# Optimization experiments

Hardware: AMD Instinct MI355X
Metric: run time of the kernel (lower is better)

## Reference

```python
import jax, jax.numpy as jnp
import numpy as np

B, LQ, NB, NT = 4, 512, 32, 256
D_MODEL, N_HEADS, D_K, D_V = 512, 8, 64, 64
SCALE = 1.0 / np.sqrt(D_K).astype(np.float32)


def setup_inputs() -> dict:
    key = jax.random.key(0)
    ks = jax.random.split(key, 16)
    std = 0.02
    p = lambda k, shp: (std * jax.random.normal(k, shp, dtype=jnp.float32))
    return {
        'q':   jax.random.normal(ks[0], (B, LQ, D_MODEL), dtype=jnp.float32),
        'k_w': jax.random.normal(ks[1], (B, NB, NT, D_MODEL), dtype=jnp.float32),
        'v_w': jax.random.normal(ks[2], (B, NB, NT, D_MODEL), dtype=jnp.float32),
        'k_s': jax.random.normal(ks[3], (B, NB, D_MODEL), dtype=jnp.float32),
        'v_s': jax.random.normal(ks[4], (B, NB, D_MODEL), dtype=jnp.float32),
        'W_qs': p(ks[5], (D_MODEL, N_HEADS * D_K)), 'b_qs': jnp.zeros((N_HEADS * D_K,), jnp.float32),
        'W_ks': p(ks[6], (D_MODEL, N_HEADS * D_K)), 'b_ks': jnp.zeros((N_HEADS * D_K,), jnp.float32),
        'W_vs': p(ks[7], (D_MODEL, N_HEADS * D_V)), 'b_vs': jnp.zeros((N_HEADS * D_V,), jnp.float32),
        'W_qw': p(ks[8], (D_MODEL, N_HEADS * D_K)), 'b_qw': jnp.zeros((N_HEADS * D_K,), jnp.float32),
        'W_kw': p(ks[9], (D_MODEL, N_HEADS * D_K)), 'b_kw': jnp.zeros((N_HEADS * D_K,), jnp.float32),
        'W_vw': p(ks[10], (D_MODEL, N_HEADS * D_V)), 'b_vw': jnp.zeros((N_HEADS * D_V,), jnp.float32),
        'W_fc1': p(ks[11], (N_HEADS * D_V, D_MODEL)), 'b_fc1': jnp.zeros((D_MODEL,), jnp.float32),
        'W_fc':  p(ks[12], (D_MODEL + N_HEADS * D_V, D_MODEL)), 'b_fc': jnp.zeros((D_MODEL,), jnp.float32),
    }


def reference(q, k_w, v_w, k_s, v_s,
              W_qs, b_qs, W_ks, b_ks, W_vs, b_vs,
              W_qw, b_qw, W_kw, b_kw, W_vw, b_vw,
              W_fc1, b_fc1, W_fc, b_fc):
    b, lq = q.shape[0], q.shape[1]
    nb, nt = k_w.shape[1], k_w.shape[2]
    h, dk, dv = N_HEADS, D_K, D_V

    # ---- sentence-level (graph) attention ----
    qs = (q @ W_qs + b_qs).reshape(b, lq, h, dk)        # [b,lq,h,dk]
    ks_ = (k_s @ W_ks + b_ks).reshape(b, nb, h, dk)     # [b,nb,h,dk]
    vs_ = (v_s @ W_vs + b_vs).reshape(b, nb, h, dv)     # [b,nb,h,dv]
    attn_s = jnp.einsum('bqhd,bnhd->bhqn', qs * SCALE, ks_)  # [b,h,lq,nb]
    attn_s = jax.nn.softmax(attn_s, axis=-1)
    ctx_s = jnp.einsum('bhqn,bnhd->bqhd', attn_s, vs_).reshape(b, lq, h * dv)
    ctx_s = ctx_s @ W_fc1 + b_fc1                        # [b,lq,d_model]

    # ---- token-level attention with sentence norm ----
    qw = (q @ W_qw + b_qw).reshape(b, lq, h, dk)         # [b,lq,h,dk]
    kw = (k_w @ W_kw + b_kw).reshape(b, nb, nt, h, dk)
    vw = (v_w @ W_vw + b_vw).reshape(b, nb, nt, h, dv)
    attn_w = jnp.einsum('bqhd,bnthd->bhqnt', qw * SCALE, kw)  # [b,h,lq,nb,nt]
    wts = jax.nn.softmax(attn_w, axis=-1)                # softmax over tokens within each block
    aw = wts * attn_s[..., None]                         # sentence-weighted token attention
    ctx_w = jnp.einsum('bhqnt,bnthd->bqhd', aw, vw).reshape(b, lq, h * dv)

    out = jnp.concatenate([ctx_s, ctx_w], axis=-1) @ W_fc + b_fc  # [b,lq,d_model]
    return out
```

## Files before the change

### kernel.cpp

```cpp
#include <hip/hip_runtime.h>
#include <hip/hip_bf16.h>

#define SCALE_F 0.125f

typedef __attribute__((ext_vector_type(8))) short short8;
typedef __attribute__((ext_vector_type(4))) float f32x4;
typedef __attribute__((address_space(3))) void lds_void;
typedef const __attribute__((address_space(1))) void glb_void;

__device__ __forceinline__ unsigned short f2b(float f){
  return __builtin_bit_cast(unsigned short, __float2bfloat16(f));
}
__device__ __forceinline__ float b2f(unsigned short h){
  return __uint_as_float((unsigned int)h << 16);
}

template<int MODE>
__device__ __forceinline__ void sgemm_body(
    unsigned short* sm, const float* __restrict__ A,
    const float* __restrict__ p0, const float* __restrict__ p1,
    const float* __restrict__ W, const float* __restrict__ bias,
    float* __restrict__ outf, float scale, int m0, int n0, int K, int tid)
{
  unsigned short* Ah = sm;
  unsigned short* Al = sm + 4096;
  unsigned short* Bh = sm + 8192;
  unsigned short* Bl = sm + 12288;
  const int lane = tid & 63, wv = tid >> 6, lr = lane & 15, lg = lane >> 4;

  f32x4 acc[4];
  #pragma unroll
  for (int nf = 0; nf < 4; nf++) acc[nf] = (f32x4){0.f, 0.f, 0.f, 0.f};

  for (int k0 = 0; k0 < K; k0 += 64) {
    float4 a0[2], a1[2];
    float bw[2][8];
    const bool dual = (MODE == 1) && (k0 >= 512);
    const int kk = dual ? (k0 - 512) : k0;
    #pragma unroll
    for (int j = 0; j < 2; j++) {
      int idx = tid + j * 256;
      int row = idx >> 3, c8 = idx & 7;
      size_t base = (size_t)(m0 + row) * 512 + kk + c8 * 8;
      if (dual) {
        float4 x0 = *(const float4*)&p0[base];
        float4 x1 = *(const float4*)&p0[base + 4];
        float4 y0 = *(const float4*)&p1[base];
        float4 y1 = *(const float4*)&p1[base + 4];
        a0[j] = (float4){x0.x + y0.x, x0.y + y0.y, x0.z + y0.z, x0.w + y0.w};
        a1[j] = (float4){x1.x + y1.x, x1.y + y1.y, x1.z + y1.z, x1.w + y1.w};
      } else {
        a0[j] = *(const float4*)&A[base];
        a1[j] = *(const float4*)&A[base + 4];
      }
    }
    #pragma unroll
    for (int j = 0; j < 2; j++) {
      int idx = tid + j * 256;
      int nl = idx >> 3, kseg = idx & 7;
      #pragma unroll
      for (int e = 0; e < 8; e++)
        bw[j][e] = W[(size_t)(k0 + kseg * 8 + e) * 512 + n0 + nl];
    }
    __syncthreads();
    #pragma unroll
    for (int j = 0; j < 2; j++) {
      int idx = tid + j * 256;
      int row = idx >> 3, c8 = idx & 7;
      int off = row * 64 + ((c8 * 8) ^ ((row & 7) << 3));
      float v[8] = {a0[j].x, a0[j].y, a0[j].z, a0[j].w,
                    a1[j].x, a1[j].y, a1[j].z, a1[j].w};
      short8 h, l;
      #pragma unroll
      for (int e = 0; e < 8; e++) {
        unsigned short hh = f2b(v[e]);
        h[e] = (short)hh;
        l[e] = (short)f2b(v[e] - b2f(hh));
      }
      *(short8*)&Ah[off] = h;
      *(short8*)&Al[off] = l;
    }
    #pragma unroll
    for (int j = 0; j < 2; j++) {
      int idx = tid + j * 256;
      int nl = idx >> 3, kseg = idx & 7;
      int off = nl * 64 + ((kseg * 8) ^ ((nl & 7) << 3));
      short8 h, l;
      #pragma unroll
      for (int e = 0; e < 8; e++) {
        unsigned short hh = f2b(bw[j][e]);
        h[e] = (short)hh;
        l[e] = (short)f2b(bw[j][e] - b2f(hh));
      }
      *(short8*)&Bh[off] = h;
      *(short8*)&Bl[off] = l;
    }
    __syncthreads();
    #pragma unroll
    for (int ks = 0; ks < 2; ks++) {
      int rowa = wv * 16 + lr;
      int aoff = rowa * 64 + ((ks * 32 + lg * 8) ^ ((rowa & 7) << 3));
      short8 ah = *(const short8*)&Ah[aoff];
      short8 al = *(const short8*)&Al[aoff];
      #pragma unroll
      for (int nf = 0; nf < 4; nf++) {
        int rowb = nf * 16 + lr;
        int boff = rowb * 64 + ((ks * 32 + lg * 8) ^ ((rowb & 7) << 3));
        short8 bh = *(const short8*)&Bh[boff];
        short8 bl = *(const short8*)&Bl[boff];
        acc[nf] = __builtin_amdgcn_mfma_f32_16x16x32_bf16(ah, bh, acc[nf], 0, 0, 0);
        acc[nf] = __builtin_amdgcn_mfma_f32_16x16x32_bf16(ah, bl, acc[nf], 0, 0, 0);
        acc[nf] = __builtin_amdgcn_mfma_f32_16x16x32_bf16(al, bh, acc[nf], 0, 0, 0);
      }
    }
  }

  #pragma unroll
  for (int nf = 0; nf < 4; nf++) {
    int n = n0 + nf * 16 + lr;
    float bv = bias[n];
    #pragma unroll
    for (int i = 0; i < 4; i++) {
      int m = m0 + wv * 16 + lg * 4 + i;
      float v = (acc[nf][i] + bv) * scale;
      if (MODE == 0 || MODE == 1) {
        outf[(size_t)m * 512 + n] = v;
      } else if (MODE == 2) {
        int bb = m >> 9, qq = m & 511, hh = n >> 6, d = n & 63;
        outf[((((size_t)bb * 8 + hh) * 512 + qq) << 6) + d] = v;
      } else {
        int bb = m >> 5, nn = m & 31, hh = n >> 6, d = n & 63;
        outf[((((size_t)bb * 8 + hh) * 32 + nn) << 6) + d] = v;
      }
    }
  }
}

template<int VT>
__device__ __forceinline__ void proj_epilogue(
    f32x4 (&acc)[4][4], const float* __restrict__ bias,
    __hip_bfloat16* __restrict__ outW, int m0, int n0,
    int wr, int wc, int lr, int lg)
{
  #pragma unroll
  for (int nj = 0; nj < 4; nj++) {
    int n = n0 + wc * 64 + nj * 16 + lr;
    float bv = bias[n];
    int hh = n >> 6, d = n & 63;
    #pragma unroll
    for (int mi = 0; mi < 4; mi++) {
      if (VT == 0) {
        #pragma unroll
        for (int i = 0; i < 4; i++) {
          int m = m0 + wr * 64 + mi * 16 + lg * 4 + i;
          int bb = m >> 13, r = m & 8191, nn = r >> 8, tt = r & 255;
          outW[(((((size_t)bb * 8 + hh) * 32 + nn) * 256 + tt) << 6) + d] =
              __float2bfloat16(acc[mi][nj][i] + bv);
        }
      } else {
        int m = m0 + wr * 64 + mi * 16 + lg * 4;
        int bb = m >> 13, r = m & 8191, nn = r >> 8, t0 = r & 255;
        uint2 pk;
        pk.x = (unsigned)f2b(acc[mi][nj][0] + bv) | ((unsigned)f2b(acc[mi][nj][1] + bv) << 16);
        pk.y = (unsigned)f2b(acc[mi][nj][2] + bv) | ((unsigned)f2b(acc[mi][nj][3] + bv) << 16);
        *(uint2*)((unsigned short*)outW +
                  (((((size_t)bb * 8 + hh) * 32 + nn) * 64 + d) << 8) + t0) = pk;
      }
    }
  }
}

template<int VT>
__device__ __forceinline__ void proj_reg(
    unsigned short* sm, const float* __restrict__ A,
    const unsigned short* __restrict__ BT, const float* __restrict__ bias,
    __hip_bfloat16* __restrict__ outW, int bidLocal, int tid)
{
  unsigned short* As = sm;
  unsigned short* Bs = sm + 8192;
  const int xcd = bidLocal & 7, local = bidLocal >> 3;
  const int mx = xcd * 32 + (local >> 2);
  const int ny = local & 3;
  const int m0 = mx * 128, n0 = ny * 128;
  const int lane = tid & 63, wv = tid >> 6, lr = lane & 15, lg = lane >> 4;
  const int wr = wv >> 1, wc = wv & 1;

  f32x4 acc[4][4];
  #pragma unroll
  for (int mi = 0; mi < 4; mi++)
    #pragma unroll
    for (int nj = 0; nj < 4; nj++) acc[mi][nj] = (f32x4){0.f, 0.f, 0.f, 0.f};

  for (int k0 = 0; k0 < 512; k0 += 64) {
    float4 a0[4], a1[4]; uint4 bq[4];
    #pragma unroll
    for (int j = 0; j < 4; j++) {
      int idx = tid + j * 256;
      int row = idx >> 3, c8 = idx & 7;
      const float* ap = A + (size_t)(m0 + row) * 512 + k0 + c8 * 8;
      a0[j] = *(const float4*)ap;
      a1[j] = *(const float4*)(ap + 4);
      bq[j] = *(const uint4*)(BT + (size_t)(n0 + row) * 512 + k0 + c8 * 8);
    }
    __syncthreads();
    #pragma unroll
    for (int j = 0; j < 4; j++) {
      int idx = tid + j * 256;
      int row = idx >> 3, c8 = idx & 7;
      int off = row * 64 + ((c8 * 8) ^ ((row & 7) << 3));
      short8 pk;
      pk[0] = (short)f2b(a0[j].x); pk[1] = (short)f2b(a0[j].y);
      pk[2] = (short)f2b(a0[j].z); pk[3] = (short)f2b(a0[j].w);
      pk[4] = (short)f2b(a1[j].x); pk[5] = (short)f2b(a1[j].y);
      pk[6] = (short)f2b(a1[j].z); pk[7] = (short)f2b(a1[j].w);
      *(short8*)&As[off] = pk;
      *(uint4*)&Bs[off] = bq[j];
    }
    __syncthreads();
    #pragma unroll
    for (int ks = 0; ks < 2; ks++) {
      short8 af[4], bfp[4];
      #pragma unroll
      for (int mi = 0; mi < 4; mi++) {
        int row = wr * 64 + mi * 16 + lr;
        af[mi] = *(const short8*)&As[row * 64 + ((ks * 32 + lg * 8) ^ ((row & 7) << 3))];
      }
      #pragma unroll
      for (int nj = 0; nj < 4; nj++) {
        int row = wc * 64 + nj * 16 + lr;
        bfp[nj] = *(const short8*)&Bs[row * 64 + ((ks * 32 + lg * 8) ^ ((row & 7) << 3))];
      }
      #pragma unroll
      for (int mi = 0; mi < 4; mi++)
        #pragma unroll
        for (int nj = 0; nj < 4; nj++)
          acc[mi][nj] = __builtin_amdgcn_mfma_f32_16x16x32_bf16(af[mi], bfp[nj], acc[mi][nj], 0, 0, 0);
    }
  }
  proj_epilogue<VT>(acc, bias, outW, m0, n0, wr, wc, lr, lg);
}

template<int VT>
__device__ __forceinline__ void proj_glds(
    unsigned short* sm, const unsigned short* __restrict__ Abf,
    const unsigned short* __restrict__ BT, const float* __restrict__ bias,
    __hip_bfloat16* __restrict__ outW, int bidLocal, int tid)
{
  unsigned short* As = sm;
  unsigned short* Bs = sm + 8192;
  const int xcd = bidLocal & 7, local = bidLocal >> 3;
  const int mx = xcd * 32 + (local >> 2);
  const int ny = local & 3;
  const int m0 = mx * 128, n0 = ny * 128;
  const int lane = tid & 63, wv = tid >> 6, lr = lane & 15, lg = lane >> 4;
  const int wr = wv >> 1, wc = wv & 1;
  const int srow = tid >> 3, scc = tid & 7;

  f32x4 acc[4][4];
  #pragma unroll
  for (int mi = 0; mi < 4; mi++)
    #pragma unroll
    for (int nj = 0; nj < 4; nj++) acc[mi][nj] = (f32x4){0.f, 0.f, 0.f, 0.f};

  for (int k0 = 0; k0 < 512; k0 += 64) {
    __syncthreads();
    #pragma unroll
    for (int issue = 0; issue < 4; issue++) {
      int row = issue * 32 + srow;
      int cs = (scc ^ (row & 7)) * 8;
      const unsigned short* ga = Abf + (size_t)(m0 + row) * 512 + k0 + cs;
      const unsigned short* gb = BT  + (size_t)(n0 + row) * 512 + k0 + cs;
      unsigned short* la = As + issue * 2048 + wv * 512;
      unsigned short* lb = Bs + issue * 2048 + wv * 512;
      __builtin_amdgcn_global_load_lds((glb_void*)ga, (lds_void*)la, 16, 0, 0);
      __builtin_amdgcn_global_load_lds((glb_void*)gb, (lds_void*)lb, 16, 0, 0);
    }
    asm volatile("s_waitcnt vmcnt(0)" ::: "memory");
    __syncthreads();
    #pragma unroll
    for (int ks = 0; ks < 2; ks++) {
      short8 af[4], bfp[4];
      #pragma unroll
      for (int mi = 0; mi < 4; mi++) {
        int row = wr * 64 + mi * 16 + lr;
        af[mi] = *(const short8*)&As[row * 64 + ((ks * 32 + lg * 8) ^ ((row & 7) << 3))];
      }
      #pragma unroll
      for (int nj = 0; nj < 4; nj++) {
        int row = wc * 64 + nj * 16 + lr;
        bfp[nj] = *(const short8*)&Bs[row * 64 + ((ks * 32 + lg * 8) ^ ((row & 7) << 3))];
      }
      #pragma unroll
      for (int mi = 0; mi < 4; mi++)
        #pragma unroll
        for (int nj = 0; nj < 4; nj++)
          acc[mi][nj] = __builtin_amdgcn_mfma_f32_16x16x32_bf16(af[mi], bfp[nj], acc[mi][nj], 0, 0, 0);
    }
  }
  proj_epilogue<VT>(acc, bias, outW, m0, n0, wr, wc, lr, lg);
}

__device__ __forceinline__ void tok_body(
    unsigned short* sm, const float* __restrict__ qw,
    const __hip_bfloat16* __restrict__ kw, const __hip_bfloat16* __restrict__ vwT,
    const float* __restrict__ attn_s, float* __restrict__ part0,
    float* __restrict__ part1, int bid, int tid)
{
  unsigned short* kvbuf = sm;
  unsigned short* pbuf  = sm + 18432;
  const int xcd = bid & 7, slot = bid >> 3;
  const int bh = xcd * 4 + (slot >> 4);
  const int rest = slot & 15;
  const int qt = rest >> 1, z = rest & 1;
  const int b = bh >> 3, h = bh & 7;
  const int wv = tid >> 6, lane = tid & 63, lg = lane >> 4, lr = lane & 15;
  const int qbase = qt * 64 + wv * 16;
  const int n0 = z * 16;
  const int vd = wv * 16 + (lane >> 2), tq = lane & 3;

  short8 qfrag[2];
  {
    const float* qrow = qw + ((size_t)bh * 512 + qbase + lr) * 64;
    #pragma unroll
    for (int ks = 0; ks < 2; ks++) {
      float4 u0 = *(const float4*)&qrow[ks * 32 + lg * 8];
      float4 u1 = *(const float4*)&qrow[ks * 32 + lg * 8 + 4];
      short8 t;
      t[0] = f2b(u0.x); t[1] = f2b(u0.y); t[2] = f2b(u0.z); t[3] = f2b(u0.w);
      t[4] = f2b(u1.x); t[5] = f2b(u1.y); t[6] = f2b(u1.z); t[7] = f2b(u1.w);
      qfrag[ks] = t;
    }
  }
  float asv[16];
  {
    const float* ap = attn_s + ((size_t)bh * 512 + qbase + lr) * 32 + n0;
    #pragma unroll
    for (int i = 0; i < 4; i++) {
      float4 u = *(const float4*)&ap[i * 4];
      asv[i * 4 + 0] = u.x; asv[i * 4 + 1] = u.y;
      asv[i * 4 + 2] = u.z; asv[i * 4 + 3] = u.w;
    }
  }

  f32x4 acc[4];
  #pragma unroll
  for (int dt = 0; dt < 4; dt++) acc[dt] = (f32x4){0.f, 0.f, 0.f, 0.f};

  const unsigned short* kwb = (const unsigned short*)kw + (size_t)bh * 32 * 256 * 64;
  const unsigned short* vtb = (const unsigned short*)vwT + (size_t)bh * 32 * 64 * 256;
  const unsigned int pbase = (wv * 16 + lr) * 264;

  for (int ni = 0; ni < 16; ni++) {
    const int n = n0 + ni;
    __syncthreads();
    {
      const unsigned short* ksrc = kwb + ((size_t)n * 256 + tid) * 64;
      uint4 r[8];
      #pragma unroll
      for (int j = 0; j < 8; j++) r[j] = *(const uint4*)(ksrc + j * 8);
      #pragma unroll
      for (int j = 0; j < 8; j++) *(uint4*)&kvbuf[tid * 72 + j * 8] = r[j];
    }
    __syncthreads();

    f32x4 sfr[16];
    #pragma unroll
    for (int tt = 0; tt < 16; tt++) sfr[tt] = (f32x4){0.f, 0.f, 0.f, 0.f};
    __builtin_amdgcn_s_setprio(1);
    #pragma unroll
    for (int tt = 0; tt < 16; tt++) {
      #pragma unroll
      for (int ks = 0; ks < 2; ks++) {
        short8 kf = *(const short8*)&kvbuf[(16 * tt + lr) * 72 + ks * 32 + lg * 8];
        sfr[tt] = __builtin_amdgcn_mfma_f32_16x16x32_bf16(kf, qfrag[ks], sfr[tt], 0, 0, 0);
      }
    }
    __builtin_amdgcn_s_setprio(0);
    float lsum = 0.f;
    #pragma unroll
    for (int tt = 0; tt < 16; tt++) {
      #pragma unroll
      for (int i = 0; i < 4; i++) {
        float e = __expf(sfr[tt][i]);
        sfr[tt][i] = e;
        lsum += e;
      }
    }
    lsum += __shfl_xor(lsum, 16);
    lsum += __shfl_xor(lsum, 32);
    const float coef = asv[ni] / lsum;
    #pragma unroll
    for (int tt = 0; tt < 16; tt++) {
      uint2 pk;
      pk.x = (unsigned)f2b(sfr[tt][0] * coef) | ((unsigned)f2b(sfr[tt][1] * coef) << 16);
      pk.y = (unsigned)f2b(sfr[tt][2] * coef) | ((unsigned)f2b(sfr[tt][3] * coef) << 16);
      *(uint2*)&pbuf[pbase + tt * 16 + lg * 4] = pk;
    }
    __syncthreads();

    {
      const unsigned short* vsrc = vtb + ((size_t)n * 64 + vd) * 256 + tq * 64;
      uint4 r[8];
      #pragma unroll
      for (int j = 0; j < 8; j++) r[j] = *(const uint4*)(vsrc + j * 8);
      #pragma unroll
      for (int j = 0; j < 8; j++)
        *(uint4*)&kvbuf[vd * 264 + tq * 64 + ((j ^ tq) * 8)] = r[j];
    }
    __syncthreads();

    __builtin_amdgcn_s_setprio(1);
    #pragma unroll
    for (int ks = 0; ks < 8; ks++) {
      short8 pa = *(const short8*)&pbuf[pbase + ks * 32 + lg * 8];
      const int tqe = ks >> 1, joff = (ks & 1) * 4 + lg;
      #pragma unroll
      for (int dt = 0; dt < 4; dt++) {
        short8 vb = *(const short8*)&kvbuf[(16 * dt + lr) * 264 + tqe * 64 + ((joff ^ tqe) * 8)];
        acc[dt] = __builtin_amdgcn_mfma_f32_16x16x32_bf16(pa, vb, acc[dt], 0, 0, 0);
      }
    }
    __builtin_amdgcn_s_setprio(0);
  }

  float* pout = z ? part1 : part0;
  #pragma unroll
  for (int dt = 0; dt < 4; dt++) {
    #pragma unroll
    for (int i = 0; i < 4; i++) {
      int qg = qt * 64 + wv * 16 + lg * 4 + i;
      pout[((size_t)b * 512 + qg) * 512 + h * 64 + dt * 16 + lr] = acc[dt][i];
    }
  }
}

__global__ __launch_bounds__(256)
void prep(const float* __restrict__ kwf, const float* __restrict__ vwf,
          unsigned short* __restrict__ kbf, unsigned short* __restrict__ vbf,
          const float* __restrict__ W0, unsigned short* __restrict__ T0,
          const float* __restrict__ W1, unsigned short* __restrict__ T1,
          int ncast)
{
  __shared__ unsigned short tile[64][72];
  const int bid = blockIdx.x, tid = threadIdx.x;
  if (bid < 2 * ncast) {
    const float* src = (bid < ncast) ? kwf : vwf;
    unsigned short* dst = (bid < ncast) ? kbf : vbf;
    size_t off = (size_t)((bid < ncast) ? bid : bid - ncast) * 8192;
    #pragma unroll
    for (int i = 0; i < 8; i++) {
      size_t idx = off + ((size_t)i * 256 + tid) * 4;
      float4 v = *(const float4*)&src[idx];
      uint2 pk;
      pk.x = (unsigned)f2b(v.x) | ((unsigned)f2b(v.y) << 16);
      pk.y = (unsigned)f2b(v.z) | ((unsigned)f2b(v.w) << 16);
      *(uint2*)&dst[idx] = pk;
    }
  } else {
    int local = bid - 2 * ncast;
    const float* W = (local >> 6) ? W1 : W0;
    unsigned short* T = (local >> 6) ? T1 : T0;
    int k0 = (local & 7) * 64, n0 = ((local >> 3) & 7) * 64;
    #pragma unroll
    for (int j = 0; j < 16; j++) {
      int idx = tid + j * 256;
      int r = idx >> 6, c = idx & 63;
      tile[r][c] = f2b(W[(size_t)(k0 + r) * 512 + n0 + c]);
    }
    __syncthreads();
    #pragma unroll
    for (int j = 0; j < 16; j++) {
      int idx = tid + j * 256;
      int r = idx >> 6, c = idx & 63;
      T[(size_t)(n0 + r) * 512 + k0 + c] = tile[c][r];
    }
  }
}

__global__ __launch_bounds__(256)
void megaA_glds(const float* __restrict__ q,
           const unsigned short* __restrict__ kbf, const unsigned short* __restrict__ vbf,
           const float* __restrict__ k_s, const float* __restrict__ v_s,
           const float* __restrict__ W_qs, const float* __restrict__ b_qs,
           const float* __restrict__ W_qw, const float* __restrict__ b_qw,
           const float* __restrict__ W_ks, const float* __restrict__ b_ks,
           const float* __restrict__ W_vs, const float* __restrict__ b_vs,
           const unsigned short* __restrict__ WkT, const float* __restrict__ b_kw,
           const unsigned short* __restrict__ WvT, const float* __restrict__ b_vw,
           float* qs_ws, float* qw_ws, float* ks_ws, float* vs_ws,
           __hip_bfloat16* kw_ws, __hip_bfloat16* vwT_ws)
{
  __shared__ unsigned short sm[16384];
  const int bid = blockIdx.x, tid = threadIdx.x;
  if (bid < 1024) {
    proj_glds<0>(sm, kbf, WkT, b_kw, kw_ws, bid, tid);
  } else if (bid < 2048) {
    proj_glds<1>(sm, vbf, WvT, b_vw, vwT_ws, bid - 1024, tid);
  } else if (bid < 2560) {
    int local = bid - 2048;
    int bx = local & 31, by = (local >> 5) & 7, bz = local >> 8;
    if (bz == 0)
      sgemm_body<2>(sm, q, nullptr, nullptr, W_qs, b_qs, qs_ws, SCALE_F, bx * 64, by * 64, 512, tid);
    else
      sgemm_body<2>(sm, q, nullptr, nullptr, W_qw, b_qw, qw_ws, SCALE_F, bx * 64, by * 64, 512, tid);
  } else {
    int local = bid - 2560;
    int bx = local & 1, by = (local >> 1) & 7, bz = local >> 4;
    if (bz == 0)
      sgemm_body<3>(sm, k_s, nullptr, nullptr, W_ks, b_ks, ks_ws, 1.f, bx * 64, by * 64, 512, tid);
    else
      sgemm_body<3>(sm, v_s, nullptr, nullptr, W_vs, b_vs, vs_ws, 1.f, bx * 64, by * 64, 512, tid);
  }
}

__global__ __launch_bounds__(256)
void megaA_reg(const float* __restrict__ q,
           const float* __restrict__ k_w, const float* __restrict__ v_w,
           const float* __restrict__ k_s, const float* __restrict__ v_s,
           const float* __restrict__ W_qs, const float* __restrict__ b_qs,
           const float* __restrict__ W_qw, const float* __restrict__ b_qw,
           const float* __restrict__ W_ks, const float* __restrict__ b_ks,
           const float* __restrict__ W_vs, const float* __restrict__ b_vs,
           const unsigned short* __restrict__ WkT, const float* __restrict__ b_kw,
           const unsigned short* __restrict__ WvT, const float* __restrict__ b_vw,
           float* qs_ws, float* qw_ws, float* ks_ws, float* vs_ws,
           __hip_bfloat16* kw_ws, __hip_bfloat16* vwT_ws)
{
  __shared__ unsigned short sm[16384];
  const int bid = blockIdx.x, tid = threadIdx.x;
  if (bid < 1024) {
    proj_reg<0>(sm, k_w, WkT, b_kw, kw_ws, bid, tid);
  } else if (bid < 2048) {
    proj_reg<1>(sm, v_w, WvT, b_vw, vwT_ws, bid - 1024, tid);
  } else if (bid < 2560) {
    int local = bid - 2048;
    int bx = local & 31, by = (local >> 5) & 7, bz = local >> 8;
    if (bz == 0)
      sgemm_body<2>(sm, q, nullptr, nullptr, W_qs, b_qs, qs_ws, SCALE_F, bx * 64, by * 64, 512, tid);
    else
      sgemm_body<2>(sm, q, nullptr, nullptr, W_qw, b_qw, qw_ws, SCALE_F, bx * 64, by * 64, 512, tid);
  } else {
    int local = bid - 2560;
    int bx = local & 1, by = (local >> 1) & 7, bz = local >> 4;
    if (bz == 0)
      sgemm_body<3>(sm, k_s, nullptr, nullptr, W_ks, b_ks, ks_ws, 1.f, bx * 64, by * 64, 512, tid);
    else
      sgemm_body<3>(sm, v_s, nullptr, nullptr, W_vs, b_vs, vs_ws, 1.f, bx * 64, by * 64, 512, tid);
  }
}

__global__ __launch_bounds__(256, 2)
void megaB(const float* __restrict__ qw,
           const __hip_bfloat16* __restrict__ kw, const __hip_bfloat16* __restrict__ vwT,
           const float* __restrict__ attn_s, float* part0, float* part1,
           const float* __restrict__ ctxs,
           const float* __restrict__ W_fc1, const float* __restrict__ b_fc1,
           float* ctxsf)
{
  __shared__ unsigned short sm[35328];
  const int bid = blockIdx.x, tid = threadIdx.x;
  if (bid < 512) {
    tok_body(sm, qw, kw, vwT, attn_s, part0, part1, bid, tid);
  } else {
    int local = bid - 512;
    sgemm_body<0>(sm, ctxs, nullptr, nullptr, W_fc1, b_fc1, ctxsf, 1.f,
                  (local & 31) * 64, (local >> 5) * 64, 512, tid);
  }
}

__global__ __launch_bounds__(256)
void final_gemm(const float* __restrict__ ctxsf,
                const float* __restrict__ p0, const float* __restrict__ p1,
                const float* __restrict__ W, const float* __restrict__ bias,
                float* out)
{
  __shared__ unsigned short sm[16384];
  sgemm_body<1>(sm, ctxsf, p0, p1, W, bias, out, 1.f,
                blockIdx.x * 64, blockIdx.y * 64, 1024, threadIdx.x);
}

__global__ __launch_bounds__(256)
void sent_attn(const float* __restrict__ qs,
               const float* __restrict__ ks,
               const float* __restrict__ vs,
               float* __restrict__ attn_s,
               float* __restrict__ ctx_s)
{
  __shared__ float qsS[32][68];
  __shared__ float ksS[32][68];
  __shared__ float vsS[32][68];
  __shared__ float sS[32][36];
  const int bh = blockIdx.y, b = bh >> 3, h = bh & 7;
  const int q0 = blockIdx.x * 32;
  const int tid = threadIdx.x;

  #pragma unroll
  for (int i = 0; i < 2; i++) {
    int idx = tid + i * 256;
    int r = idx >> 4, c = (idx & 15) * 4;
    *(float4*)&qsS[r][c] = *(const float4*)&qs[((size_t)bh * 512 + q0 + r) * 64 + c];
    *(float4*)&ksS[r][c] = *(const float4*)&ks[((size_t)bh * 32 + r) * 64 + c];
    *(float4*)&vsS[r][c] = *(const float4*)&vs[((size_t)bh * 32 + r) * 64 + c];
  }
  __syncthreads();

  #pragma unroll
  for (int it = 0; it < 4; it++) {
    int pair = tid + it * 256;
    int qq = pair >> 5, nn = pair & 31;
    float s = 0.f;
    #pragma unroll
    for (int k = 0; k < 64; k++) s += qsS[qq][k] * ksS[nn][k];
    sS[qq][nn] = s;
  }
  __syncthreads();

  if (tid < 32) {
    int qq = tid;
    float m = -1e30f;
    #pragma unroll
    for (int n = 0; n < 32; n++) m = fmaxf(m, sS[qq][n]);
    float p[32];
    float sum = 0.f;
    #pragma unroll
    for (int n = 0; n < 32; n++) { p[n] = __expf(sS[qq][n] - m); sum += p[n]; }
    float inv = 1.f / sum;
    #pragma unroll
    for (int n = 0; n < 32; n++) {
      float pv = p[n] * inv;
      sS[qq][n] = pv;
      attn_s[((size_t)bh * 512 + q0 + qq) * 32 + n] = pv;
    }
  }
  __syncthreads();

  #pragma unroll
  for (int it = 0; it < 8; it++) {
    int idx = tid + it * 256;
    int qq = idx >> 6, d = idx & 63;
    float c = 0.f;
    #pragma unroll
    for (int n = 0; n < 32; n++) c += sS[qq][n] * vsS[n][d];
    ctx_s[((size_t)b * 512 + q0 + qq) * 512 + h * 64 + d] = c;
  }
}

extern "C" void kernel_launch(void* const* d_in, const int* in_sizes, int n_in,
                              void* d_out, int out_size, void* d_ws, size_t ws_size,
                              hipStream_t stream)
{
  (void)in_sizes; (void)n_in; (void)out_size;
  const float* q    = (const float*)d_in[0];
  const float* k_w  = (const float*)d_in[1];
  const float* v_w  = (const float*)d_in[2];
  const float* k_s  = (const float*)d_in[3];
  const float* v_s  = (const float*)d_in[4];
  const float* W_qs = (const float*)d_in[5];  const float* b_qs = (const float*)d_in[6];
  const float* W_ks = (const float*)d_in[7];  const float* b_ks = (const float*)d_in[8];
  const float* W_vs = (const float*)d_in[9];  const float* b_vs = (const float*)d_in[10];
  const float* W_qw = (const float*)d_in[11]; const float* b_qw = (const float*)d_in[12];
  const float* W_kw = (const float*)d_in[13]; const float* b_kw = (const float*)d_in[14];
  const float* W_vw = (const float*)d_in[15]; const float* b_vw = (const float*)d_in[16];
  const float* W_fc1= (const float*)d_in[17]; const float* b_fc1= (const float*)d_in[18];
  const float* W_fc = (const float*)d_in[19]; const float* b_fc = (const float*)d_in[20];
  float* out = (float*)d_out;

  char* ws = (char*)d_ws;
  const size_t MB = 1ull << 20;
  const size_t KB = 1ull << 10;
  float* qs_ws    = (float*)(ws + 0 * MB);
  float* qw_ws    = (float*)(ws + 4 * MB);
  float* ks_ws    = (float*)(ws + 8 * MB);
  unsigned short* WkT = (unsigned short*)(ws + 8 * MB + 512 * KB);
  float* vs_ws    = (float*)(ws + 9 * MB);
  unsigned short* WvT = (unsigned short*)(ws + 9 * MB + 512 * KB);
  float* attns_ws = (float*)(ws + 10 * MB);
  float* ctxs_ws  = (float*)(ws + 12 * MB);
  float* ctxsf_ws = (float*)(ws + 16 * MB);
  float* part1    = (float*)(ws + 20 * MB);
  __hip_bfloat16* kw_ws  = (__hip_bfloat16*)(ws + 24 * MB);
  __hip_bfloat16* vwT_ws = (__hip_bfloat16*)(ws + 56 * MB);
  unsigned short* kbf = (unsigned short*)(ws + 88 * MB);
  unsigned short* vbf = (unsigned short*)(ws + 120 * MB);
  float* part0    = (float*)(ws + 0 * MB);

  const bool use_glds = (ws_size >= 152ull * MB);
  const int ncast = use_glds ? 2048 : 0;

  dim3 blk(256);
  prep<<<dim3(2 * ncast + 128), blk, 0, stream>>>(
      k_w, v_w, kbf, vbf, W_kw, WkT, W_vw, WvT, ncast);
  if (use_glds) {
    megaA_glds<<<dim3(2592), blk, 0, stream>>>(
        q, kbf, vbf, k_s, v_s,
        W_qs, b_qs, W_qw, b_qw, W_ks, b_ks, W_vs, b_vs,
        WkT, b_kw, WvT, b_vw,
        qs_ws, qw_ws, ks_ws, vs_ws, kw_ws, vwT_ws);
  } else {
    megaA_reg<<<dim3(2592), blk, 0, stream>>>(
        q, k_w, v_w, k_s, v_s,
        W_qs, b_qs, W_qw, b_qw, W_ks, b_ks, W_vs, b_vs,
        WkT, b_kw, WvT, b_vw,
        qs_ws, qw_ws, ks_ws, vs_ws, kw_ws, vwT_ws);
  }
  sent_attn<<<dim3(16, 32), blk, 0, stream>>>(qs_ws, ks_ws, vs_ws, attns_ws, ctxs_ws);
  megaB<<<dim3(768), blk, 0, stream>>>(
      qw_ws, kw_ws, vwT_ws, attns_ws, part0, part1,
      ctxs_ws, W_fc1, b_fc1, ctxsf_ws);
  final_gemm<<<dim3(32, 8), blk, 0, stream>>>(ctxsf_ws, part0, part1, W_fc, b_fc, out);
}
```

Baseline: 271.1 us.

## Regroup kernels: fold small projections into cast prep, sentence attention into K/V projection

The q/k_s/v_s projections move out of the big K/V projection kernel into the first prep kernel, next to the bf16 casts and the weight transposes. Sentence attention, which only depends on those projections, now runs as extra blocks inside the K/V projection kernel, so one launch disappears. Separately, the token-attention LDS buffers switch from padded rows to XOR-swizzled unpadded layouts, which shrinks megaB shared memory to 64KB and aims to avoid bank conflicts. The risks are load imbalance from the heterogeneous block mixes and correctness of the new swizzle indexing.

```diff
diff --git a/kernel.cpp b/kernel.cpp
--- a/kernel.cpp
+++ b/kernel.cpp
@@ -300,6 +300,69 @@
   proj_epilogue<VT>(acc, bias, outW, m0, n0, wr, wc, lr, lg);
 }
 
+__device__ __forceinline__ void sent_body(
+    float* smf, const float* __restrict__ qs, const float* __restrict__ ks,
+    const float* __restrict__ vs, float* __restrict__ attn_s,
+    float* __restrict__ ctx_s, int bidLocal, int tid)
+{
+  float* qsS = smf;
+  float* ksS = smf + 2176;
+  float* vsS = smf + 4352;
+  float* sS  = smf + 6528;
+  const int bh = bidLocal >> 4, b = bh >> 3, h = bh & 7;
+  const int q0 = (bidLocal & 15) * 32;
+
+  #pragma unroll
+  for (int i = 0; i < 2; i++) {
+    int idx = tid + i * 256;
+    int r = idx >> 4, c = (idx & 15) * 4;
+    *(float4*)&qsS[r * 68 + c] = *(const float4*)&qs[((size_t)bh * 512 + q0 + r) * 64 + c];
+    *(float4*)&ksS[r * 68 + c] = *(const float4*)&ks[((size_t)bh * 32 + r) * 64 + c];
+    *(float4*)&vsS[r * 68 + c] = *(const float4*)&vs[((size_t)bh * 32 + r) * 64 + c];
+  }
+  __syncthreads();
+
+  #pragma unroll
+  for (int it = 0; it < 4; it++) {
+    int pair = tid + it * 256;
+    int qq = pair >> 5, nn = pair & 31;
+    float s = 0.f;
+    #pragma unroll
+    for (int k = 0; k < 64; k++) s += qsS[qq * 68 + k] * ksS[nn * 68 + k];
+    sS[qq * 36 + nn] = s;
+  }
+  __syncthreads();
+
+  if (tid < 32) {
+    int qq = tid;
+    float m = -1e30f;
+    #pragma unroll
+    for (int n = 0; n < 32; n++) m = fmaxf(m, sS[qq * 36 + n]);
+    float p[32];
+    float sum = 0.f;
+    #pragma unroll
+    for (int n = 0; n < 32; n++) { p[n] = __expf(sS[qq * 36 + n] - m); sum += p[n]; }
+    float inv = 1.f / sum;
+    #pragma unroll
+    for (int n = 0; n < 32; n++) {
+      float pv = p[n] * inv;
+      sS[qq * 36 + n] = pv;
+      attn_s[((size_t)bh * 512 + q0 + qq) * 32 + n] = pv;
+    }
+  }
+  __syncthreads();
+
+  #pragma unroll
+  for (int it = 0; it < 8; it++) {
+    int idx = tid + it * 256;
+    int qq = idx >> 6, d = idx & 63;
+    float c = 0.f;
+    #pragma unroll
+    for (int n = 0; n < 32; n++) c += sS[qq * 36 + n] * vsS[n * 68 + d];
+    ctx_s[((size_t)b * 512 + q0 + qq) * 512 + h * 64 + d] = c;
+  }
+}
+
 __device__ __forceinline__ void tok_body(
     unsigned short* sm, const float* __restrict__ qw,
     const __hip_bfloat16* __restrict__ kw, const __hip_bfloat16* __restrict__ vwT,
@@ -307,7 +370,7 @@
     float* __restrict__ part1, int bid, int tid)
 {
   unsigned short* kvbuf = sm;
-  unsigned short* pbuf  = sm + 18432;
+  unsigned short* pbuf  = sm + 16384;
   const int xcd = bid & 7, slot = bid >> 3;
   const int bh = xcd * 4 + (slot >> 4);
   const int rest = slot & 15;
@@ -317,6 +380,8 @@
   const int qbase = qt * 64 + wv * 16;
   const int n0 = z * 16;
   const int vd = wv * 16 + (lane >> 2), tq = lane & 3;
+  const int swz = (lr & 7) << 3;
+  const int vswz = (vd & 7) << 3;
 
   short8 qfrag[2];
   {
@@ -348,7 +413,7 @@
 
   const unsigned short* kwb = (const unsigned short*)kw + (size_t)bh * 32 * 256 * 64;
   const unsigned short* vtb = (const unsigned short*)vwT + (size_t)bh * 32 * 64 * 256;
-  const unsigned int pbase = (wv * 16 + lr) * 264;
+  const unsigned int prow = (wv * 16 + lr) * 256;
 
   for (int ni = 0; ni < 16; ni++) {
     const int n = n0 + ni;
@@ -359,7 +424,8 @@
       #pragma unroll
       for (int j = 0; j < 8; j++) r[j] = *(const uint4*)(ksrc + j * 8);
       #pragma unroll
-      for (int j = 0; j < 8; j++) *(uint4*)&kvbuf[tid * 72 + j * 8] = r[j];
+      for (int j = 0; j < 8; j++)
+        *(uint4*)&kvbuf[tid * 64 + (((j << 3)) ^ ((tid & 7) << 3))] = r[j];
     }
     __syncthreads();
 
@@ -371,7 +437,7 @@
     for (int tt = 0; tt < 16; tt++) {
       #pragma unroll
       for (int ks = 0; ks < 2; ks++) {
-        short8 kf = *(const short8*)&kvbuf[(16 * tt + lr) * 72 + ks * 32 + lg * 8];
+        short8 kf = *(const short8*)&kvbuf[(16 * tt + lr) * 64 + ((ks * 32 + lg * 8) ^ swz)];
         sfr[tt] = __builtin_amdgcn_mfma_f32_16x16x32_bf16(kf, qfrag[ks], sfr[tt], 0, 0, 0);
       }
     }
@@ -394,7 +460,7 @@
       uint2 pk;
       pk.x = (unsigned)f2b(sfr[tt][0] * coef) | ((unsigned)f2b(sfr[tt][1] * coef) << 16);
       pk.y = (unsigned)f2b(sfr[tt][2] * coef) | ((unsigned)f2b(sfr[tt][3] * coef) << 16);
-      *(uint2*)&pbuf[pbase + tt * 16 + lg * 4] = pk;
+      *(uint2*)&pbuf[prow + ((((tt * 2 + (lg >> 1)) << 3) ^ swz) | ((lg & 1) << 2))] = pk;
     }
     __syncthreads();
 
@@ -405,18 +471,17 @@
       for (int j = 0; j < 8; j++) r[j] = *(const uint4*)(vsrc + j * 8);
       #pragma unroll
       for (int j = 0; j < 8; j++)
-        *(uint4*)&kvbuf[vd * 264 + tq * 64 + ((j ^ tq) * 8)] = r[j];
+        *(uint4*)&kvbuf[vd * 256 + ((((tq * 8 + j) << 3)) ^ vswz)] = r[j];
     }
     __syncthreads();
 
     __builtin_amdgcn_s_setprio(1);
     #pragma unroll
     for (int ks = 0; ks < 8; ks++) {
-      short8 pa = *(const short8*)&pbuf[pbase + ks * 32 + lg * 8];
-      const int tqe = ks >> 1, joff = (ks & 1) * 4 + lg;
+      short8 pa = *(const short8*)&pbuf[prow + ((ks * 32 + lg * 8) ^ swz)];
       #pragma unroll
       for (int dt = 0; dt < 4; dt++) {
-        short8 vb = *(const short8*)&kvbuf[(16 * dt + lr) * 264 + tqe * 64 + ((joff ^ tqe) * 8)];
+        short8 vb = *(const short8*)&kvbuf[(16 * dt + lr) * 256 + ((ks * 32 + lg * 8) ^ swz)];
         acc[dt] = __builtin_amdgcn_mfma_f32_16x16x32_bf16(pa, vb, acc[dt], 0, 0, 0);
       }
     }
@@ -435,18 +500,57 @@
 }
 
 __global__ __launch_bounds__(256)
-void prep(const float* __restrict__ kwf, const float* __restrict__ vwf,
-          unsigned short* __restrict__ kbf, unsigned short* __restrict__ vbf,
-          const float* __restrict__ W0, unsigned short* __restrict__ T0,
-          const float* __restrict__ W1, unsigned short* __restrict__ T1,
-          int ncast)
-{
-  __shared__ unsigned short tile[64][72];
+void megaQ(const float* __restrict__ q,
+           const float* __restrict__ k_s, const float* __restrict__ v_s,
+           const float* __restrict__ W_qs, const float* __restrict__ b_qs,
+           const float* __restrict__ W_qw, const float* __restrict__ b_qw,
+           const float* __restrict__ W_ks, const float* __restrict__ b_ks,
+           const float* __restrict__ W_vs, const float* __restrict__ b_vs,
+           const float* __restrict__ kwf, const float* __restrict__ vwf,
+           unsigned short* __restrict__ kbf, unsigned short* __restrict__ vbf,
+           const float* __restrict__ W_kw, unsigned short* __restrict__ WkT,
+           const float* __restrict__ W_vw, unsigned short* __restrict__ WvT,
+           float* qs_ws, float* qw_ws, float* ks_ws, float* vs_ws, int ncast)
+{
+  __shared__ __attribute__((aligned(16))) unsigned short sm[16384];
   const int bid = blockIdx.x, tid = threadIdx.x;
-  if (bid < 2 * ncast) {
-    const float* src = (bid < ncast) ? kwf : vwf;
-    unsigned short* dst = (bid < ncast) ? kbf : vbf;
-    size_t off = (size_t)((bid < ncast) ? bid : bid - ncast) * 8192;
+  if (bid < 512) {
+    int bx = bid & 31, by = (bid >> 5) & 7, bz = bid >> 8;
+    if (bz == 0)
+      sgemm_body<2>(sm, q, nullptr, nullptr, W_qs, b_qs, qs_ws, SCALE_F, bx * 64, by * 64, 512, tid);
+    else
+      sgemm_body<2>(sm, q, nullptr, nullptr, W_qw, b_qw, qw_ws, SCALE_F, bx * 64, by * 64, 512, tid);
+  } else if (bid < 544) {
+    int local = bid - 512;
+    int bx = local & 1, by = (local >> 1) & 7, bz = local >> 4;
+    if (bz == 0)
+      sgemm_body<3>(sm, k_s, nullptr, nullptr, W_ks, b_ks, ks_ws, 1.f, bx * 64, by * 64, 512, tid);
+    else
+      sgemm_body<3>(sm, v_s, nullptr, nullptr, W_vs, b_vs, vs_ws, 1.f, bx * 64, by * 64, 512, tid);
+  } else if (bid < 672) {
+    int local = bid - 544;
+    const float* W = (local >> 6) ? W_vw : W_kw;
+    unsigned short* T = (local >> 6) ? WvT : WkT;
+    int k0 = (local & 7) * 64, n0 = ((local >> 3) & 7) * 64;
+    unsigned short* tile = sm;
+    #pragma unroll
+    for (int j = 0; j < 16; j++) {
+      int idx = tid + j * 256;
+      int r = idx >> 6, c = idx & 63;
+      tile[r * 72 + c] = f2b(W[(size_t)(k0 + r) * 512 + n0 + c]);
+    }
+    __syncthreads();
+    #pragma unroll
+    for (int j = 0; j < 16; j++) {
+      int idx = tid + j * 256;
+      int r = idx >> 6, c = idx & 63;
+      T[(size_t)(n0 + r) * 512 + k0 + c] = tile[c * 72 + r];
+    }
+  } else {
+    int local = bid - 672;
+    const float* src = (local < ncast) ? kwf : vwf;
+    unsigned short* dst = (local < ncast) ? kbf : vbf;
+    size_t off = (size_t)((local < ncast) ? local : local - ncast) * 8192;
     #pragma unroll
     for (int i = 0; i < 8; i++) {
       size_t idx = off + ((size_t)i * 256 + tid) * 4;
@@ -456,96 +560,45 @@
       pk.y = (unsigned)f2b(v.z) | ((unsigned)f2b(v.w) << 16);
       *(uint2*)&dst[idx] = pk;
     }
-  } else {
-    int local = bid - 2 * ncast;
-    const float* W = (local >> 6) ? W1 : W0;
-    unsigned short* T = (local >> 6) ? T1 : T0;
-    int k0 = (local & 7) * 64, n0 = ((local >> 3) & 7) * 64;
-    #pragma unroll
-    for (int j = 0; j < 16; j++) {
-      int idx = tid + j * 256;
-      int r = idx >> 6, c = idx & 63;
-      tile[r][c] = f2b(W[(size_t)(k0 + r) * 512 + n0 + c]);
-    }
-    __syncthreads();
-    #pragma unroll
-    for (int j = 0; j < 16; j++) {
-      int idx = tid + j * 256;
-      int r = idx >> 6, c = idx & 63;
-      T[(size_t)(n0 + r) * 512 + k0 + c] = tile[c][r];
-    }
   }
 }
 
 __global__ __launch_bounds__(256)
-void megaA_glds(const float* __restrict__ q,
-           const unsigned short* __restrict__ kbf, const unsigned short* __restrict__ vbf,
-           const float* __restrict__ k_s, const float* __restrict__ v_s,
-           const float* __restrict__ W_qs, const float* __restrict__ b_qs,
-           const float* __restrict__ W_qw, const float* __restrict__ b_qw,
-           const float* __restrict__ W_ks, const float* __restrict__ b_ks,
-           const float* __restrict__ W_vs, const float* __restrict__ b_vs,
-           const unsigned short* __restrict__ WkT, const float* __restrict__ b_kw,
-           const unsigned short* __restrict__ WvT, const float* __restrict__ b_vw,
-           float* qs_ws, float* qw_ws, float* ks_ws, float* vs_ws,
-           __hip_bfloat16* kw_ws, __hip_bfloat16* vwT_ws)
-{
-  __shared__ unsigned short sm[16384];
+void megaP_glds(const unsigned short* __restrict__ kbf,
+                const unsigned short* __restrict__ vbf,
+                const unsigned short* __restrict__ WkT, const float* __restrict__ b_kw,
+                const unsigned short* __restrict__ WvT, const float* __restrict__ b_vw,
+                __hip_bfloat16* kw_ws, __hip_bfloat16* vwT_ws,
+                const float* __restrict__ qs, const float* __restrict__ ks,
+                const float* __restrict__ vs, float* attn_s, float* ctx_s)
+{
+  __shared__ __attribute__((aligned(16))) unsigned short sm[16384];
   const int bid = blockIdx.x, tid = threadIdx.x;
   if (bid < 1024) {
     proj_glds<0>(sm, kbf, WkT, b_kw, kw_ws, bid, tid);
   } else if (bid < 2048) {
     proj_glds<1>(sm, vbf, WvT, b_vw, vwT_ws, bid - 1024, tid);
-  } else if (bid < 2560) {
-    int local = bid - 2048;
-    int bx = local & 31, by = (local >> 5) & 7, bz = local >> 8;
-    if (bz == 0)
-      sgemm_body<2>(sm, q, nullptr, nullptr, W_qs, b_qs, qs_ws, SCALE_F, bx * 64, by * 64, 512, tid);
-    else
-      sgemm_body<2>(sm, q, nullptr, nullptr, W_qw, b_qw, qw_ws, SCALE_F, bx * 64, by * 64, 512, tid);
   } else {
-    int local = bid - 2560;
-    int bx = local & 1, by = (local >> 1) & 7, bz = local >> 4;
-    if (bz == 0)
-      sgemm_body<3>(sm, k_s, nullptr, nullptr, W_ks, b_ks, ks_ws, 1.f, bx * 64, by * 64, 512, tid);
-    else
-      sgemm_body<3>(sm, v_s, nullptr, nullptr, W_vs, b_vs, vs_ws, 1.f, bx * 64, by * 64, 512, tid);
+    sent_body((float*)sm, qs, ks, vs, attn_s, ctx_s, bid - 2048, tid);
   }
 }
 
 __global__ __launch_bounds__(256)
-void megaA_reg(const float* __restrict__ q,
-           const float* __restrict__ k_w, const float* __restrict__ v_w,
-           const float* __restrict__ k_s, const float* __restrict__ v_s,
-           const float* __restrict__ W_qs, const float* __restrict__ b_qs,
-           const float* __restrict__ W_qw, const float* __restrict__ b_qw,
-           const float* __restrict__ W_ks, const float* __restrict__ b_ks,
-           const float* __restrict__ W_vs, const float* __restrict__ b_vs,
-           const unsigned short* __restrict__ WkT, const float* __restrict__ b_kw,
-           const unsigned short* __restrict__ WvT, const float* __restrict__ b_vw,
-           float* qs_ws, float* qw_ws, float* ks_ws, float* vs_ws,
-           __hip_bfloat16* kw_ws, __hip_bfloat16* vwT_ws)
-{
-  __shared__ unsigned short sm[16384];
+void megaP_reg(const float* __restrict__ k_w, const float* __restrict__ v_w,
+               const unsigned short* __restrict__ WkT, const float* __restrict__ b_kw,
+               const unsigned short* __restrict__ WvT, const float* __restrict__ b_vw,
+               __hip_bfloat16* kw_ws, __hip_bfloat16* vwT_ws,
+               const float* __restrict__ qs, const float* __restrict__ ks,
+               const float* __restrict__ vs, float* attn_s, float* ctx_s)
+{
+  __shared__ __attribute__((aligned(16))) unsigned short sm[16384];
   const int bid = blockIdx.x, tid = threadIdx.x;
   if (bid < 1024) {
     proj_reg<0>(sm, k_w, WkT, b_kw, kw_ws, bid, tid);
   } else if (bid < 2048) {
     proj_reg<1>(sm, v_w, WvT, b_vw, vwT_ws, bid - 1024, tid);
-  } else if (bid < 2560) {
-    int local = bid - 2048;
-    int bx = local & 31, by = (local >> 5) & 7, bz = local >> 8;
-    if (bz == 0)
-      sgemm_body<2>(sm, q, nullptr, nullptr, W_qs, b_qs, qs_ws, SCALE_F, bx * 64, by * 64, 512, tid);
-    else
-      sgemm_body<2>(sm, q, nullptr, nullptr, W_qw, b_qw, qw_ws, SCALE_F, bx * 64, by * 64, 512, tid);
   } else {
-    int local = bid - 2560;
-    int bx = local & 1, by = (local >> 1) & 7, bz = local >> 4;
-    if (bz == 0)
-      sgemm_body<3>(sm, k_s, nullptr, nullptr, W_ks, b_ks, ks_ws, 1.f, bx * 64, by * 64, 512, tid);
-    else
-      sgemm_body<3>(sm, v_s, nullptr, nullptr, W_vs, b_vs, vs_ws, 1.f, bx * 64, by * 64, 512, tid);
+    sent_body((float*)sm, qs, ks, vs, attn_s, ctx_s, bid - 2048, tid);
   }
 }
 
@@ -557,7 +610,7 @@
            const float* __restrict__ W_fc1, const float* __restrict__ b_fc1,
            float* ctxsf)
 {
-  __shared__ unsigned short sm[35328];
+  __shared__ __attribute__((aligned(16))) unsigned short sm[32768];
   const int bid = blockIdx.x, tid = threadIdx.x;
   if (bid < 512) {
     tok_body(sm, qw, kw, vwT, attn_s, part0, part1, bid, tid);
@@ -574,75 +627,9 @@
                 const float* __restrict__ W, const float* __restrict__ bias,
                 float* out)
 {
-  __shared__ unsigned short sm[16384];
+  __shared__ __attribute__((aligned(16))) unsigned short sm[16384];
   sgemm_body<1>(sm, ctxsf, p0, p1, W, bias, out, 1.f,
                 blockIdx.x * 64, blockIdx.y * 64, 1024, threadIdx.x);
-}
-
-__global__ __launch_bounds__(256)
-void sent_attn(const float* __restrict__ qs,
-               const float* __restrict__ ks,
-               const float* __restrict__ vs,
-               float* __restrict__ attn_s,
-               float* __restrict__ ctx_s)
-{
-  __shared__ float qsS[32][68];
-  __shared__ float ksS[32][68];
-  __shared__ float vsS[32][68];
-  __shared__ float sS[32][36];
-  const int bh = blockIdx.y, b = bh >> 3, h = bh & 7;
-  const int q0 = blockIdx.x * 32;
-  const int tid = threadIdx.x;
-
-  #pragma unroll
-  for (int i = 0; i < 2; i++) {
-    int idx = tid + i * 256;
-    int r = idx >> 4, c = (idx & 15) * 4;
-    *(float4*)&qsS[r][c] = *(const float4*)&qs[((size_t)bh * 512 + q0 + r) * 64 + c];
-    *(float4*)&ksS[r][c] = *(const float4*)&ks[((size_t)bh * 32 + r) * 64 + c];
-    *(float4*)&vsS[r][c] = *(const float4*)&vs[((size_t)bh * 32 + r) * 64 + c];
-  }
-  __syncthreads();
-
-  #pragma unroll
-  for (int it = 0; it < 4; it++) {
-    int pair = tid + it * 256;
-    int qq = pair >> 5, nn = pair & 31;
-    float s = 0.f;
-    #pragma unroll
-    for (int k = 0; k < 64; k++) s += qsS[qq][k] * ksS[nn][k];
-    sS[qq][nn] = s;
-  }
-  __syncthreads();
-
-  if (tid < 32) {
-    int qq = tid;
-    float m = -1e30f;
-    #pragma unroll
-    for (int n = 0; n < 32; n++) m = fmaxf(m, sS[qq][n]);
-    float p[32];
-    float sum = 0.f;
-    #pragma unroll
-    for (int n = 0; n < 32; n++) { p[n] = __expf(sS[qq][n] - m); sum += p[n]; }
-    float inv = 1.f / sum;
-    #pragma unroll
-    for (int n = 0; n < 32; n++) {
-      float pv = p[n] * inv;
-      sS[qq][n] = pv;
-      attn_s[((size_t)bh * 512 + q0 + qq) * 32 + n] = pv;
-    }
-  }
-  __syncthreads();
-
-  #pragma unroll
-  for (int it = 0; it < 8; it++) {
-    int idx = tid + it * 256;
-    int qq = idx >> 6, d = idx & 63;
-    float c = 0.f;
-    #pragma unroll
-    for (int n = 0; n < 32; n++) c += sS[qq][n] * vsS[n][d];
-    ctx_s[((size_t)b * 512 + q0 + qq) * 512 + h * 64 + d] = c;
-  }
 }
 
 extern "C" void kernel_launch(void* const* d_in, const int* in_sizes, int n_in,
@@ -688,22 +675,19 @@
   const int ncast = use_glds ? 2048 : 0;
 
   dim3 blk(256);
-  prep<<<dim3(2 * ncast + 128), blk, 0, stream>>>(
-      k_w, v_w, kbf, vbf, W_kw, WkT, W_vw, WvT, ncast);
+  megaQ<<<dim3(672 + 2 * ncast), blk, 0, stream>>>(
+      q, k_s, v_s, W_qs, b_qs, W_qw, b_qw, W_ks, b_ks, W_vs, b_vs,
+      k_w, v_w, kbf, vbf, W_kw, WkT, W_vw, WvT,
+      qs_ws, qw_ws, ks_ws, vs_ws, ncast);
   if (use_glds) {
-    megaA_glds<<<dim3(2592), blk, 0, stream>>>(
-        q, kbf, vbf, k_s, v_s,
-        W_qs, b_qs, W_qw, b_qw, W_ks, b_ks, W_vs, b_vs,
-        WkT, b_kw, WvT, b_vw,
-        qs_ws, qw_ws, ks_ws, vs_ws, kw_ws, vwT_ws);
+    megaP_glds<<<dim3(2560), blk, 0, stream>>>(
+        kbf, vbf, WkT, b_kw, WvT, b_vw, kw_ws, vwT_ws,
+        qs_ws, ks_ws, vs_ws, attns_ws, ctxs_ws);
   } else {
-    megaA_reg<<<dim3(2592), blk, 0, stream>>>(
-        q, k_w, v_w, k_s, v_s,
-        W_qs, b_qs, W_qw, b_qw, W_ks, b_ks, W_vs, b_vs,
-        WkT, b_kw, WvT, b_vw,
-        qs_ws, qw_ws, ks_ws, vs_ws, kw_ws, vwT_ws);
-  }
-  sent_attn<<<dim3(16, 32), blk, 0, stream>>>(qs_ws, ks_ws, vs_ws, attns_ws, ctxs_ws);
+    megaP_reg<<<dim3(2560), blk, 0, stream>>>(
+        k_w, v_w, WkT, b_kw, WvT, b_vw, kw_ws, vwT_ws,
+        qs_ws, ks_ws, vs_ws, attns_ws, ctxs_ws);
+  }
   megaB<<<dim3(768), blk, 0, stream>>>(
       qw_ws, kw_ws, vwT_ws, attns_ws, part0, part1,
       ctxs_ws, W_fc1, b_fc1, ctxsf_ws);
```

New measurement: 238.6 us, median of 3. 12.0% less time.
